# Performance work log

Measured on AMD Instinct MI355X. Metric: run time of the kernel, lower is better.

The kernel has to match this reference:

```python
import jax, jax.numpy as jnp
import numpy as np

N_EMBD = 768
N_HEAD = 12
HEAD_DIM = N_EMBD // N_HEAD


def setup_inputs() -> dict:
    key = jax.random.key(0)
    k0, k1, k2, k3, k4 = jax.random.split(key, 5)
    B, T, C = 2, 4096, N_EMBD
    x = jax.random.normal(k0, (B, T, C), dtype=jnp.float32)
    # c_attn: Linear(C, 3C); c_proj: Linear(C, C). torch Linear: y = x @ W.T + b
    s = 1.0 / np.sqrt(C)
    W_attn = jax.random.uniform(k1, (3 * C, C), dtype=jnp.float32, minval=-s, maxval=s)
    b_attn = jax.random.uniform(k2, (3 * C,), dtype=jnp.float32, minval=-s, maxval=s)
    W_proj = jax.random.uniform(k3, (C, C), dtype=jnp.float32, minval=-s, maxval=s)
    b_proj = jax.random.uniform(k4, (C,), dtype=jnp.float32, minval=-s, maxval=s)
    return {"x": x, "W_attn": W_attn, "b_attn": b_attn, "W_proj": W_proj, "b_proj": b_proj}


def reference(x, W_attn, b_attn, W_proj, b_proj):
    B, T, C = x.shape
    H, D = N_HEAD, HEAD_DIM
    qkv = x @ W_attn.T + b_attn                      # [B,T,3C]
    q, k, v = jnp.split(qkv, 3, axis=-1)
    # [B,T,C] -> [B,H,T,D]
    q = q.reshape(B, T, H, D).transpose(0, 2, 1, 3)
    k = k.reshape(B, T, H, D).transpose(0, 2, 1, 3)
    v = v.reshape(B, T, H, D).transpose(0, 2, 1, 3)
    scale = 1.0 / jnp.sqrt(jnp.asarray(D, dtype=x.dtype))
    att = jnp.einsum('bhqd,bhkd->bhqk', q, k) * scale  # [B,H,T,T]
    att = jax.nn.softmax(att, axis=-1)
    y = jnp.einsum('bhqk,bhkd->bhqd', att, v)          # [B,H,T,D]
    y = y.transpose(0, 2, 1, 3).reshape(B, T, C)
    return y @ W_proj.T + b_proj
```

## Files before the change

### kernel.cpp

```cpp
#include <hip/hip_runtime.h>
#include <stdint.h>
#include <stddef.h>

typedef __bf16 bf16_t;
typedef bf16_t bf16x4 __attribute__((ext_vector_type(4)));
typedef bf16_t bf16x8 __attribute__((ext_vector_type(8)));
typedef float  f32x4  __attribute__((ext_vector_type(4)));
typedef _Float16 f16_t;
typedef f16_t f16x2 __attribute__((ext_vector_type(2)));
typedef f16_t f16x4 __attribute__((ext_vector_type(4)));
typedef f16_t f16x8 __attribute__((ext_vector_type(8)));
typedef __fp16 fp16x2_raw __attribute__((ext_vector_type(2)));

__device__ __forceinline__ f16x2 pkrtz(float a, float b) {
    fp16x2_raw r = __builtin_amdgcn_cvt_pkrtz(a, b);
    union { fp16x2_raw r; f16x2 h; } u;
    u.r = r;
    return u.h;
}

#define MFMA_BF16_K32(a, b, c) __builtin_amdgcn_mfma_f32_16x16x32_bf16(a, b, c, 0, 0, 0)
#define MFMA_F16_K32(a, b, c)  __builtin_amdgcn_mfma_f32_16x16x32_f16(a, b, c, 0, 0, 0)

__device__ __forceinline__ void gload_lds16(const void* g, void* l) {
    __builtin_amdgcn_global_load_lds(
        (const __attribute__((address_space(1))) void*)g,
        (__attribute__((address_space(3))) void*)l,
        16, 0, 0);
}

#define NX 1572864
#define NWA 442368
#define NWP 147456
__global__ void cvt_all(const float* __restrict__ x, const float* __restrict__ Wa,
                        const float* __restrict__ Wp, bf16_t* __restrict__ xb,
                        bf16_t* __restrict__ Wab, bf16_t* __restrict__ Wpb) {
    int i = blockIdx.x * blockDim.x + threadIdx.x;
    const float4* src; bf16_t* dst; int j;
    if (i < NX)            { src = (const float4*)x;  dst = xb;  j = i; }
    else if (i < NX + NWA) { src = (const float4*)Wa; dst = Wab; j = i - NX; }
    else                   { src = (const float4*)Wp; dst = Wpb; j = i - NX - NWA; }
    float4 f = src[j];
    bf16x4 o = { (bf16_t)f.x, (bf16_t)f.y, (bf16_t)f.z, (bf16_t)f.w };
    ((bf16x4*)dst)[j] = o;
}

template <int KDIM>
__device__ __forceinline__ void gemm_mainloop(
    const bf16_t* __restrict__ A, const bf16_t* __restrict__ Bt,
    bf16_t* As, bf16_t* Bs, int m0, int n0, int wave, int lane, f32x4 acc[4][4])
{
    const int quad = lane >> 4, l15 = lane & 15;
    const int wm = ((wave >> 1) << 6), wn = ((wave & 1) << 6);

    const int srow = (wave << 4) + (lane >> 2);
    const int sw   = (((lane & 3) ^ ((srow >> 1) & 3)) << 3);
    const bf16_t* gA = A  + (size_t)(m0 + srow) * KDIM + sw;
    const bf16_t* gB = Bt + (size_t)(n0 + srow) * KDIM + sw;
    bf16_t* lA0 = As + wave * 512;
    bf16_t* lA1 = As + 2048 + wave * 512;
    bf16_t* lB0 = Bs + wave * 512;
    bf16_t* lB1 = Bs + 2048 + wave * 512;

    const int xorv = ((quad ^ ((l15 >> 1) & 3)) << 3);

    for (int k0 = 0; k0 < KDIM; k0 += 32) {
        __syncthreads();
        gload_lds16(gA + k0,                       lA0);
        gload_lds16(gA + (size_t)64 * KDIM + k0,   lA1);
        gload_lds16(gB + k0,                       lB0);
        gload_lds16(gB + (size_t)64 * KDIM + k0,   lB1);
        __syncthreads();

        bf16x8 af[4], bfr[4];
#pragma unroll
        for (int t = 0; t < 4; t++) {
            af[t]  = *(const bf16x8*)(As + (wm + t * 16 + l15) * 32 + xorv);
            bfr[t] = *(const bf16x8*)(Bs + (wn + t * 16 + l15) * 32 + xorv);
        }
#pragma unroll
        for (int mt = 0; mt < 4; mt++)
#pragma unroll
            for (int nt = 0; nt < 4; nt++)
                acc[mt][nt] = MFMA_BF16_K32(af[mt], bfr[nt], acc[mt][nt]);
    }
}

__global__ __launch_bounds__(256) void gemm_qkv(
    const bf16_t* __restrict__ A,
    const bf16_t* __restrict__ Bt,
    const float* __restrict__ bias,
    bf16_t* __restrict__ qo, bf16_t* __restrict__ ko, f16_t* __restrict__ vo)
{
    __shared__ bf16_t As[128 * 32];
    __shared__ bf16_t Bs[128 * 32];
    const int tid = threadIdx.x, wave = tid >> 6, lane = tid & 63;
    const int quad = lane >> 4, l15 = lane & 15;
    const int m0 = blockIdx.y * 128, n0 = blockIdx.x * 128;
    f32x4 acc[4][4] = {};
    gemm_mainloop<768>(A, Bt, As, Bs, m0, n0, wave, lane, acc);

    const int wm = ((wave >> 1) << 6), wn = ((wave & 1) << 6);
#pragma unroll
    for (int nt = 0; nt < 4; nt++) {
        const int cc = n0 + wn + nt * 16 + l15;
        const float bia = bias[cc];
        const int which = cc / 768;
        const int rem = cc - which * 768;
        const int h = rem >> 6, d = rem & 63;
        if (which < 2) {
            bf16_t* dst = (which == 0) ? qo : ko;
#pragma unroll
            for (int mt = 0; mt < 4; mt++) {
#pragma unroll
                for (int r = 0; r < 4; r++) {
                    const int row = m0 + wm + mt * 16 + quad * 4 + r;
                    const int b = row >> 12, t = row & 4095;
                    dst[((size_t)(b * 12 + h) * 4096 + t) * 64 + d] =
                        (bf16_t)(acc[mt][nt][r] + bia);
                }
            }
        } else {
#pragma unroll
            for (int mt = 0; mt < 4; mt++) {
                const int row0 = m0 + wm + mt * 16 + quad * 4;
                const int b = row0 >> 12, t0 = row0 & 4095;
                f16x4 ov = { (f16_t)(acc[mt][nt][0] + bia),
                             (f16_t)(acc[mt][nt][1] + bia),
                             (f16_t)(acc[mt][nt][2] + bia),
                             (f16_t)(acc[mt][nt][3] + bia) };
                *(f16x4*)(vo + ((size_t)(b * 12 + h) * 64 + d) * 4096 + t0) = ov;
            }
        }
    }
}

__global__ __launch_bounds__(256) void gemm_proj(
    const bf16_t* __restrict__ A,
    const bf16_t* __restrict__ Bt,
    const float* __restrict__ bias,
    float* __restrict__ out)
{
    __shared__ bf16_t As[128 * 32];
    __shared__ bf16_t Bs[128 * 32];
    const int tid = threadIdx.x, wave = tid >> 6, lane = tid & 63;
    const int quad = lane >> 4, l15 = lane & 15;
    const int m0 = blockIdx.y * 128, n0 = blockIdx.x * 128;
    f32x4 acc[4][4] = {};
    gemm_mainloop<768>(A, Bt, As, Bs, m0, n0, wave, lane, acc);

    const int wm = ((wave >> 1) << 6), wn = ((wave & 1) << 6);
#pragma unroll
    for (int nt = 0; nt < 4; nt++) {
        const int cc = n0 + wn + nt * 16 + l15;
        const float bia = bias[cc];
#pragma unroll
        for (int mt = 0; mt < 4; mt++) {
#pragma unroll
            for (int r = 0; r < 4; r++) {
                const int row = m0 + wm + mt * 16 + quad * 4 + r;
                out[(size_t)row * 768 + cc] = acc[mt][nt][r] + bia;
            }
        }
    }
}

#define QSCALE 0.1803368801f
#define SBAR()   __builtin_amdgcn_s_barrier()
#define SCHEDB() __builtin_amdgcn_sched_barrier(0)
#define WAITV(N) asm volatile("s_waitcnt vmcnt(" #N ")" ::: "memory")
__global__ __launch_bounds__(256, 3) void attn_fwd(
    const bf16_t* __restrict__ qg, const bf16_t* __restrict__ kg,
    const f16_t* __restrict__ vtg, bf16_t* __restrict__ y)
{
    __shared__ __align__(16) char smem[36864];
    bf16_t* Ks0 = (bf16_t*)(smem);
    bf16_t* Ks1 = (bf16_t*)(smem + 8192);
    f16_t*  Vt0 = (f16_t*)(smem + 16384);
    f16_t*  Vt1 = (f16_t*)(smem + 24576);
    float*  RedA = (float*)(smem);
    float*  RedB = (float*)(smem + 17408);
    float*  Psr  = (float*)(smem + 34816);
    float*  PsT  = (float*)(smem + 35840);

    const int tid = threadIdx.x, wave = tid >> 6, lane = tid & 63;
    const int quad = lane >> 4, l15 = lane & 15;

    const int blk = blockIdx.x;
    const int xcd = blk & 7;
    const int idx = blk >> 3;
    const int hl  = idx % 3;
    const int qt  = idx / 3;
    const int bh  = xcd * 3 + hl;
    const int b = bh / 12, h = bh - b * 12;
    const size_t base = (size_t)bh * 4096 * 64;

    bf16x8 qf[4][2];
#pragma unroll
    for (int qc = 0; qc < 4; qc++) {
        const int qrow = qt * 64 + qc * 16 + l15;
        qf[qc][0] = *(const bf16x8*)(qg + base + (size_t)qrow * 64 + quad * 8);
        qf[qc][1] = *(const bf16x8*)(qg + base + (size_t)qrow * 64 + 32 + quad * 8);
#pragma unroll
        for (int j = 0; j < 8; j++) {
            qf[qc][0][j] = (bf16_t)((float)qf[qc][0][j] * QSCALE);
            qf[qc][1][j] = (bf16_t)((float)qf[qc][1][j] * QSCALE);
        }
    }

    f32x4 O[4][4] = {};
    f32x4 PS[4] = {};
    f16x8 ones8;
#pragma unroll
    for (int j = 0; j < 8; j++) ones8[j] = (f16_t)1.0f;

    const int srow8 = tid >> 3;
    const int sc8   = (tid & 7) ^ (srow8 & 7);
    const int l8 = l15 & 7;
    const int w16 = wave << 4;
    const int ksoff = (quad ^ l8) << 3;
    const int vslot = ((wave << 1) | (quad >> 1)) ^ l8;
    const int q0off = (quad & 1) * 8;

    auto stage_k = [&](const bf16_t* kp_, bf16_t* Kd) {
#pragma unroll
        for (int i = 0; i < 2; i++)
            gload_lds16(kp_ + (i * 32 + srow8) * 64 + sc8 * 8, Kd + (i * 256 + tid) * 8);
    };
    auto stage_v = [&](const f16_t* vp_, f16_t* Vd) {
#pragma unroll
        for (int i = 0; i < 2; i++)
            gload_lds16(vp_ + (size_t)(i * 32 + srow8) * 4096 + sc8 * 8, Vd + (i * 256 + tid) * 8);
    };

    const bf16_t* kp = kg + base;
    const f16_t*  vp = vtg + base;
    stage_k(kp, Ks0); stage_k(kp + 4096, Ks1);
    stage_v(vp, Vt0); stage_v(vp + 64, Vt1);
    __syncthreads();

    for (int p = 0; p < 32; p++) {
        const bf16_t* krA = Ks0 + (w16 + l15) * 64;
        const bf16_t* krB = Ks1 + (w16 + l15) * 64;
        bf16x8 kfA0 = *(const bf16x8*)(krA + ksoff);
        bf16x8 kfA1 = *(const bf16x8*)(krA + (ksoff ^ 32));
        bf16x8 kfB0 = *(const bf16x8*)(krB + ksoff);
        bf16x8 kfB1 = *(const bf16x8*)(krB + (ksoff ^ 32));
        f32x4 scA[4], scB[4];
        __builtin_amdgcn_s_setprio(1);
#pragma unroll
        for (int qc = 0; qc < 4; qc++) {
            f32x4 s = {};
            s = MFMA_BF16_K32(kfA0, qf[qc][0], s);
            s = MFMA_BF16_K32(kfA1, qf[qc][1], s);
            scA[qc] = s;
        }
#pragma unroll
        for (int qc = 0; qc < 4; qc++) {
            f32x4 s = {};
            s = MFMA_BF16_K32(kfB0, qf[qc][0], s);
            s = MFMA_BF16_K32(kfB1, qf[qc][1], s);
            scB[qc] = s;
        }
        __builtin_amdgcn_s_setprio(0);
        f16x8 pf8[4];
#pragma unroll
        for (int qc = 0; qc < 4; qc++) {
            float a0 = __builtin_amdgcn_exp2f(scA[qc][0]);
            float a1 = __builtin_amdgcn_exp2f(scA[qc][1]);
            float a2 = __builtin_amdgcn_exp2f(scA[qc][2]);
            float a3 = __builtin_amdgcn_exp2f(scA[qc][3]);
            float b0 = __builtin_amdgcn_exp2f(scB[qc][0]);
            float b1 = __builtin_amdgcn_exp2f(scB[qc][1]);
            float b2 = __builtin_amdgcn_exp2f(scB[qc][2]);
            float b3 = __builtin_amdgcn_exp2f(scB[qc][3]);
            f16x2 loA = pkrtz(a0, a1);
            f16x2 hiA = pkrtz(a2, a3);
            f16x2 loB = pkrtz(b0, b1);
            f16x2 hiB = pkrtz(b2, b3);
            union { f16x8 v; f16x2 h[4]; } u;
            u.h[0] = loA; u.h[1] = hiA; u.h[2] = loB; u.h[3] = hiB;
            pf8[qc] = u.v;
        }
        WAITV(0);
        SBAR();
        SCHEDB();
        if (p < 31) {
            const bf16_t* kn = kp + (size_t)(p + 1) * 8192;
            stage_k(kn, Ks0); stage_k(kn + 4096, Ks1);
        }
        __builtin_amdgcn_s_setprio(1);
#pragma unroll
        for (int dt = 0; dt < 4; dt++) {
            const char* vrA = (const char*)(Vt0 + (dt * 16 + l15) * 64);
            const char* vrB = (const char*)(Vt1 + (dt * 16 + l15) * 64);
            f16x4 vA = *(const f16x4*)(vrA + vslot * 16 + q0off);
            f16x4 vB = *(const f16x4*)(vrB + vslot * 16 + q0off);
            union { f16x8 v; f16x4 h[2]; } uv;
            uv.h[0] = vA; uv.h[1] = vB;
#pragma unroll
            for (int qc = 0; qc < 4; qc++)
                O[dt][qc] = MFMA_F16_K32(uv.v, pf8[qc], O[dt][qc]);
        }
#pragma unroll
        for (int qc = 0; qc < 4; qc++)
            PS[qc] = MFMA_F16_K32(ones8, pf8[qc], PS[qc]);
        __builtin_amdgcn_s_setprio(0);
        WAITV(0);
        SBAR();
        SCHEDB();
        if (p < 31) {
            const f16_t* vn = vp + (size_t)(p + 1) * 128;
            stage_v(vn, Vt0); stage_v(vn + 64, Vt1);
        }
    }

    __syncthreads();
    if (wave == 2) {
#pragma unroll
        for (int dt = 0; dt < 4; dt++)
#pragma unroll
            for (int qc = 0; qc < 4; qc++)
                *(f32x4*)(RedA + (qc * 16 + l15) * 68 + dt * 16 + quad * 4) = O[dt][qc];
    } else if (wave == 3) {
#pragma unroll
        for (int dt = 0; dt < 4; dt++)
#pragma unroll
            for (int qc = 0; qc < 4; qc++)
                *(f32x4*)(RedB + (qc * 16 + l15) * 68 + dt * 16 + quad * 4) = O[dt][qc];
    }
    if (quad == 0) {
#pragma unroll
        for (int qc = 0; qc < 4; qc++) Psr[wave * 64 + qc * 16 + l15] = PS[qc][0];
    }
    __syncthreads();
    if (wave == 0) {
#pragma unroll
        for (int dt = 0; dt < 4; dt++)
#pragma unroll
            for (int qc = 0; qc < 4; qc++)
                O[dt][qc] += *(const f32x4*)(RedA + (qc * 16 + l15) * 68 + dt * 16 + quad * 4);
    } else if (wave == 1) {
#pragma unroll
        for (int dt = 0; dt < 4; dt++)
#pragma unroll
            for (int qc = 0; qc < 4; qc++)
                O[dt][qc] += *(const f32x4*)(RedB + (qc * 16 + l15) * 68 + dt * 16 + quad * 4);
    }
    __syncthreads();
    if (wave == 1) {
#pragma unroll
        for (int dt = 0; dt < 4; dt++)
#pragma unroll
            for (int qc = 0; qc < 4; qc++)
                *(f32x4*)(RedA + (qc * 16 + l15) * 68 + dt * 16 + quad * 4) = O[dt][qc];
    } else if (wave == 3) {
        PsT[lane] = Psr[lane] + Psr[64 + lane] + Psr[128 + lane] + Psr[192 + lane];
    }
    __syncthreads();
    if (wave == 0) {
#pragma unroll
        for (int qc = 0; qc < 4; qc++) {
            const float rcp = 1.0f / PsT[qc * 16 + l15];
            const int t = qt * 64 + qc * 16 + l15;
            bf16_t* yr = y + ((size_t)b * 4096 + t) * 768 + h * 64 + quad * 4;
#pragma unroll
            for (int dt = 0; dt < 4; dt++) {
                f32x4 o4 = O[dt][qc] +
                    *(const f32x4*)(RedA + (qc * 16 + l15) * 68 + dt * 16 + quad * 4);
                bf16x4 ov = { (bf16_t)(o4[0] * rcp), (bf16_t)(o4[1] * rcp),
                              (bf16_t)(o4[2] * rcp), (bf16_t)(o4[3] * rcp) };
                *(bf16x4*)(yr + dt * 16) = ov;
            }
        }
    }
}

extern "C" void kernel_launch(void* const* d_in, const int* in_sizes, int n_in,
                              void* d_out, int out_size, void* d_ws, size_t ws_size,
                              hipStream_t stream) {
    const float* x  = (const float*)d_in[0];
    const float* Wa = (const float*)d_in[1];
    const float* ba = (const float*)d_in[2];
    const float* Wp = (const float*)d_in[3];
    const float* bp = (const float*)d_in[4];
    float* out = (float*)d_out;

    char* ws = (char*)d_ws;
    bf16_t* xb  = (bf16_t*)(ws);
    bf16_t* Wab = (bf16_t*)(ws + 12582912);
    bf16_t* Wpb = (bf16_t*)(ws + 16121856);
    bf16_t* qb  = (bf16_t*)(ws + 17301504);
    bf16_t* kb  = (bf16_t*)(ws + 29884416);
    f16_t*  vtb = (f16_t*)(ws + 42467328);
    bf16_t* yb  = (bf16_t*)(ws + 55050240);

    cvt_all<<<8448, 256, 0, stream>>>(x, Wa, Wp, xb, Wab, Wpb);
    gemm_qkv <<<dim3(18, 64), 256, 0, stream>>>(xb, Wab, ba, qb, kb, vtb);
    attn_fwd <<<1536, 256, 0, stream>>>(qb, kb, vtb, yb);
    gemm_proj<<<dim3( 6, 64), 256, 0, stream>>>(yb, Wpb, bp, out);
}
```

Baseline: 276.9 us.

## Double-buffer GEMM LDS staging and shrink attention reduction shared memory

The GEMM mainloop now double-buffers its A/B LDS tiles. The next k-slice is issued with global_load_lds before computing on the current one, and only one barrier is kept per iteration, so load latency overlaps MFMA work. The attention epilogue reduces the partial O across waves through a single shared buffer in more serialized steps, which cuts attention LDS from 36KB to 32KB to help occupancy. The cost is doubled GEMM LDS use and extra barriers in the attention reduction.

```diff
diff --git a/kernel.cpp b/kernel.cpp
--- a/kernel.cpp
+++ b/kernel.cpp
@@ -21,6 +21,10 @@
 
 #define MFMA_BF16_K32(a, b, c) __builtin_amdgcn_mfma_f32_16x16x32_bf16(a, b, c, 0, 0, 0)
 #define MFMA_F16_K32(a, b, c)  __builtin_amdgcn_mfma_f32_16x16x32_f16(a, b, c, 0, 0, 0)
+
+#define SBAR()   __builtin_amdgcn_s_barrier()
+#define SCHEDB() __builtin_amdgcn_sched_barrier(0)
+#define WAITV(N) asm volatile("s_waitcnt vmcnt(" #N ")" ::: "memory")
 
 __device__ __forceinline__ void gload_lds16(const void* g, void* l) {
     __builtin_amdgcn_global_load_lds(
@@ -57,26 +61,31 @@
     const int sw   = (((lane & 3) ^ ((srow >> 1) & 3)) << 3);
     const bf16_t* gA = A  + (size_t)(m0 + srow) * KDIM + sw;
     const bf16_t* gB = Bt + (size_t)(n0 + srow) * KDIM + sw;
-    bf16_t* lA0 = As + wave * 512;
-    bf16_t* lA1 = As + 2048 + wave * 512;
-    bf16_t* lB0 = Bs + wave * 512;
-    bf16_t* lB1 = Bs + 2048 + wave * 512;
-
+    const int loff = wave * 512;
     const int xorv = ((quad ^ ((l15 >> 1) & 3)) << 3);
 
-    for (int k0 = 0; k0 < KDIM; k0 += 32) {
+    auto stage = [&](int k0, int buf) {
+        bf16_t* a0 = As + buf * 4096 + loff;
+        bf16_t* b0 = Bs + buf * 4096 + loff;
+        gload_lds16(gA + k0,                     a0);
+        gload_lds16(gA + (size_t)64 * KDIM + k0, a0 + 2048);
+        gload_lds16(gB + k0,                     b0);
+        gload_lds16(gB + (size_t)64 * KDIM + k0, b0 + 2048);
+    };
+
+    stage(0, 0);
+    int buf = 0;
+    for (int k0 = 0; k0 < KDIM; k0 += 32, buf ^= 1) {
+        WAITV(0);
         __syncthreads();
-        gload_lds16(gA + k0,                       lA0);
-        gload_lds16(gA + (size_t)64 * KDIM + k0,   lA1);
-        gload_lds16(gB + k0,                       lB0);
-        gload_lds16(gB + (size_t)64 * KDIM + k0,   lB1);
-        __syncthreads();
-
+        if (k0 + 32 < KDIM) stage(k0 + 32, buf ^ 1);
+        const bf16_t* as = As + buf * 4096;
+        const bf16_t* bs = Bs + buf * 4096;
         bf16x8 af[4], bfr[4];
 #pragma unroll
         for (int t = 0; t < 4; t++) {
-            af[t]  = *(const bf16x8*)(As + (wm + t * 16 + l15) * 32 + xorv);
-            bfr[t] = *(const bf16x8*)(Bs + (wn + t * 16 + l15) * 32 + xorv);
+            af[t]  = *(const bf16x8*)(as + (wm + t * 16 + l15) * 32 + xorv);
+            bfr[t] = *(const bf16x8*)(bs + (wn + t * 16 + l15) * 32 + xorv);
         }
 #pragma unroll
         for (int mt = 0; mt < 4; mt++)
@@ -92,8 +101,8 @@
     const float* __restrict__ bias,
     bf16_t* __restrict__ qo, bf16_t* __restrict__ ko, f16_t* __restrict__ vo)
 {
-    __shared__ bf16_t As[128 * 32];
-    __shared__ bf16_t Bs[128 * 32];
+    __shared__ bf16_t As[2 * 128 * 32];
+    __shared__ bf16_t Bs[2 * 128 * 32];
     const int tid = threadIdx.x, wave = tid >> 6, lane = tid & 63;
     const int quad = lane >> 4, l15 = lane & 15;
     const int m0 = blockIdx.y * 128, n0 = blockIdx.x * 128;
@@ -141,8 +150,8 @@
     const float* __restrict__ bias,
     float* __restrict__ out)
 {
-    __shared__ bf16_t As[128 * 32];
-    __shared__ bf16_t Bs[128 * 32];
+    __shared__ bf16_t As[2 * 128 * 32];
+    __shared__ bf16_t Bs[2 * 128 * 32];
     const int tid = threadIdx.x, wave = tid >> 6, lane = tid & 63;
     const int quad = lane >> 4, l15 = lane & 15;
     const int m0 = blockIdx.y * 128, n0 = blockIdx.x * 128;
@@ -166,22 +175,18 @@
 }
 
 #define QSCALE 0.1803368801f
-#define SBAR()   __builtin_amdgcn_s_barrier()
-#define SCHEDB() __builtin_amdgcn_sched_barrier(0)
-#define WAITV(N) asm volatile("s_waitcnt vmcnt(" #N ")" ::: "memory")
 __global__ __launch_bounds__(256, 3) void attn_fwd(
     const bf16_t* __restrict__ qg, const bf16_t* __restrict__ kg,
     const f16_t* __restrict__ vtg, bf16_t* __restrict__ y)
 {
-    __shared__ __align__(16) char smem[36864];
+    __shared__ __align__(16) char smem[32768];
     bf16_t* Ks0 = (bf16_t*)(smem);
     bf16_t* Ks1 = (bf16_t*)(smem + 8192);
     f16_t*  Vt0 = (f16_t*)(smem + 16384);
     f16_t*  Vt1 = (f16_t*)(smem + 24576);
-    float*  RedA = (float*)(smem);
-    float*  RedB = (float*)(smem + 17408);
-    float*  Psr  = (float*)(smem + 34816);
-    float*  PsT  = (float*)(smem + 35840);
+    float*  Red  = (float*)(smem);
+    float*  Psr  = (float*)(smem + 17408);
+    float*  PsT  = (float*)(smem + 18432);
 
     const int tid = threadIdx.x, wave = tid >> 6, lane = tid & 63;
     const int quad = lane >> 4, l15 = lane & 15;
@@ -321,41 +326,45 @@
         for (int dt = 0; dt < 4; dt++)
 #pragma unroll
             for (int qc = 0; qc < 4; qc++)
-                *(f32x4*)(RedA + (qc * 16 + l15) * 68 + dt * 16 + quad * 4) = O[dt][qc];
-    } else if (wave == 3) {
+                *(f32x4*)(Red + (qc * 16 + l15) * 68 + dt * 16 + quad * 4) = O[dt][qc];
+    }
+    if (quad == 0) {
+#pragma unroll
+        for (int qc = 0; qc < 4; qc++) Psr[wave * 64 + qc * 16 + l15] = PS[qc][0];
+    }
+    __syncthreads();
+    if (wave == 0) {
 #pragma unroll
         for (int dt = 0; dt < 4; dt++)
 #pragma unroll
             for (int qc = 0; qc < 4; qc++)
-                *(f32x4*)(RedB + (qc * 16 + l15) * 68 + dt * 16 + quad * 4) = O[dt][qc];
-    }
-    if (quad == 0) {
-#pragma unroll
-        for (int qc = 0; qc < 4; qc++) Psr[wave * 64 + qc * 16 + l15] = PS[qc][0];
-    }
-    __syncthreads();
-    if (wave == 0) {
-#pragma unroll
-        for (int dt = 0; dt < 4; dt++)
-#pragma unroll
-            for (int qc = 0; qc < 4; qc++)
-                O[dt][qc] += *(const f32x4*)(RedA + (qc * 16 + l15) * 68 + dt * 16 + quad * 4);
-    } else if (wave == 1) {
-#pragma unroll
-        for (int dt = 0; dt < 4; dt++)
-#pragma unroll
-            for (int qc = 0; qc < 4; qc++)
-                O[dt][qc] += *(const f32x4*)(RedB + (qc * 16 + l15) * 68 + dt * 16 + quad * 4);
-    }
-    __syncthreads();
-    if (wave == 1) {
-#pragma unroll
-        for (int dt = 0; dt < 4; dt++)
-#pragma unroll
-            for (int qc = 0; qc < 4; qc++)
-                *(f32x4*)(RedA + (qc * 16 + l15) * 68 + dt * 16 + quad * 4) = O[dt][qc];
+                O[dt][qc] += *(const f32x4*)(Red + (qc * 16 + l15) * 68 + dt * 16 + quad * 4);
     } else if (wave == 3) {
         PsT[lane] = Psr[lane] + Psr[64 + lane] + Psr[128 + lane] + Psr[192 + lane];
+    }
+    __syncthreads();
+    if (wave == 3) {
+#pragma unroll
+        for (int dt = 0; dt < 4; dt++)
+#pragma unroll
+            for (int qc = 0; qc < 4; qc++)
+                *(f32x4*)(Red + (qc * 16 + l15) * 68 + dt * 16 + quad * 4) = O[dt][qc];
+    }
+    __syncthreads();
+    if (wave == 1) {
+#pragma unroll
+        for (int dt = 0; dt < 4; dt++)
+#pragma unroll
+            for (int qc = 0; qc < 4; qc++)
+                O[dt][qc] += *(const f32x4*)(Red + (qc * 16 + l15) * 68 + dt * 16 + quad * 4);
+    }
+    __syncthreads();
+    if (wave == 1) {
+#pragma unroll
+        for (int dt = 0; dt < 4; dt++)
+#pragma unroll
+            for (int qc = 0; qc < 4; qc++)
+                *(f32x4*)(Red + (qc * 16 + l15) * 68 + dt * 16 + quad * 4) = O[dt][qc];
     }
     __syncthreads();
     if (wave == 0) {
@@ -367,7 +376,7 @@
 #pragma unroll
             for (int dt = 0; dt < 4; dt++) {
                 f32x4 o4 = O[dt][qc] +
-                    *(const f32x4*)(RedA + (qc * 16 + l15) * 68 + dt * 16 + quad * 4);
+                    *(const f32x4*)(Red + (qc * 16 + l15) * 68 + dt * 16 + quad * 4);
                 bf16x4 ov = { (bf16_t)(o4[0] * rcp), (bf16_t)(o4[1] * rcp),
                               (bf16_t)(o4[2] * rcp), (bf16_t)(o4[3] * rcp) };
                 *(bf16x4*)(yr + dt * 16) = ov;
```

Measured after the change: 271.1 us. 2.1% less time.
